# Kernel optimization log

Measured on AMD Instinct MI355X. Metric: run time of the kernel, lower is better.

The kernel has to match this reference:

```python
import jax, jax.numpy as jnp
import numpy as np

N, E = 50000, 800000
IN_F, OUT_F, HID, MSG = 64, 64, 128, 64
TAU = 0.1
EPS = 1e-10


def setup_inputs() -> dict:
    key = jax.random.key(0)
    ks = jax.random.split(key, 16)
    s = 0.05
    return {
        "x": jax.random.normal(ks[0], (N, IN_F), jnp.float32),
        "z": jax.random.normal(ks[1], (N, OUT_F), jnp.float32),
        "src": jax.random.randint(ks[2], (E,), 0, N, jnp.int32),
        "dst": jax.random.randint(ks[3], (E,), 0, N, jnp.int32),
        "u": jax.random.uniform(ks[4], (E, MSG), jnp.float32),
        # f_enc: Linear(in,hid) -> ReLU -> Linear(hid,msg)
        "W_enc1": jax.random.normal(ks[5], (IN_F, HID), jnp.float32) * s,
        "b_enc1": jnp.zeros((HID,), jnp.float32),
        "W_enc2": jax.random.normal(ks[6], (HID, MSG), jnp.float32) * s,
        "b_enc2": jnp.zeros((MSG,), jnp.float32),
        # f_dec: Linear(msg,hid) -> ReLU
        "W_dec": jax.random.normal(ks[7], (MSG, HID), jnp.float32) * s,
        "b_dec": jnp.zeros((HID,), jnp.float32),
        # GRUCell(in+hid -> out): torch layout [3*out, in_dim], gate order r,z,n
        "W_ih": jax.random.normal(ks[8], (3 * OUT_F, IN_F + HID), jnp.float32) * s,
        "b_ih": jnp.zeros((3 * OUT_F,), jnp.float32),
        "W_hh": jax.random.normal(ks[9], (3 * OUT_F, OUT_F), jnp.float32) * s,
        "b_hh": jnp.zeros((3 * OUT_F,), jnp.float32),
    }


def gru_cell(inp, h, W_ih, b_ih, W_hh, b_hh):
    gi = inp @ W_ih.T + b_ih  # [N, 3*out]
    gh = h @ W_hh.T + b_hh
    i_r, i_z, i_n = jnp.split(gi, 3, axis=-1)
    h_r, h_z, h_n = jnp.split(gh, 3, axis=-1)
    r = jax.nn.sigmoid(i_r + h_r)
    zg = jax.nn.sigmoid(i_z + h_z)
    n = jnp.tanh(i_n + r * h_n)
    return (1.0 - zg) * n + zg * h


def reference(x, z, src, dst, u, W_enc1, b_enc1, W_enc2, b_enc2,
              W_dec, b_dec, W_ih, b_ih, W_hh, b_hh):
    # --- message: gather src features, encode, gumbel-softmax (soft) ---
    src_x = x[src]                                    # [E, in]
    logits = jax.nn.relu(src_x @ W_enc1 + b_enc1) @ W_enc2 + b_enc2  # [E, msg]
    g = -jnp.log(-jnp.log(u + EPS) + EPS)             # gumbel noise
    m = jax.nn.softmax((logits + g) / TAU, axis=-1)   # [E, msg]
    # --- aggregate: per-destination max over mailbox ---
    y = jax.ops.segment_max(m, dst, num_segments=N)   # [N, msg]
    y = jnp.where(jnp.isfinite(y), y, 0.0)            # zero-in-degree -> 0 (DGL default)
    # --- decode + GRU update ---
    dec = jax.nn.relu(y @ W_dec + b_dec)              # [N, hid]
    h_out = gru_cell(jnp.concatenate((x, dec), axis=1), z, W_ih, b_ih, W_hh, b_hh)
    return (h_out, h_out)
```

## Files before the change

### kernel.cpp

```cpp
#include <hip/hip_runtime.h>
#include <stdint.h>

#define N_NODES 50000
#define E_EDGES 800000

typedef float f32x4 __attribute__((ext_vector_type(4)));
typedef short s16x8 __attribute__((ext_vector_type(8)));
typedef unsigned short u16x8 __attribute__((ext_vector_type(8)));

__device__ inline unsigned short f2bf(float f) {
    unsigned int u = __float_as_uint(f);
    return (unsigned short)((u + 0x7FFFu + ((u >> 16) & 1u)) >> 16);
}

__device__ inline f32x4 mfma16(s16x8 a, s16x8 b, f32x4 c) {
    return __builtin_amdgcn_mfma_f32_16x16x32_bf16(a, b, c, 0, 0, 0);
}

__global__ void convert_weights(const float* __restrict__ W_enc1, const float* __restrict__ W_enc2,
                                const float* __restrict__ W_dec, const float* __restrict__ W_ih,
                                const float* __restrict__ W_hh, short* __restrict__ wf) {
    int i = blockIdx.x * 256 + threadIdx.x;
    if (i >= 73728) return;
    int j = i & 7, lane = (i >> 3) & 63, g = i >> 9;
    int l15 = lane & 15, q = lane >> 4;
    float v;
    if (g < 16) {
        int gg = g, kk = gg & 1, t = gg >> 1;
        int n = t * 16 + l15, k = kk * 32 + q * 8 + j;
        v = W_enc1[k * 128 + n];
    } else if (g < 32) {
        int gg = g - 16, kk = gg & 3, t = gg >> 2;
        int n = t * 16 + l15, k = kk * 32 + q * 8 + j;
        v = W_enc2[k * 64 + n];
    } else if (g < 48) {
        int gg = g - 32, kk = gg & 1, t = gg >> 1;
        int n = t * 16 + l15, k = kk * 32 + q * 8 + j;
        v = W_dec[k * 128 + n];
    } else if (g < 120) {
        int gg = g - 48, kk = gg % 6, t = gg / 6;
        int n = t * 16 + l15, k = kk * 32 + q * 8 + j;
        v = W_ih[n * 192 + k];
    } else {
        int gg = g - 120, kk = gg & 1, t = gg >> 1;
        int n = t * 16 + l15, k = kk * 32 + q * 8 + j;
        v = W_hh[n * 64 + k];
    }
    wf[i] = f2bf(v);
}

__global__ __launch_bounds__(256) void encoder_kernel(
    const float* __restrict__ x, const float* __restrict__ bs1, const float* __restrict__ bs2,
    const short* __restrict__ W1f, const short* __restrict__ W2f,
    unsigned short* __restrict__ lgb, float* __restrict__ y) {
    __shared__ short sA[64 * 66];
    __shared__ short sH[64 * 130];
    const int tid = threadIdx.x;
    const int nbase = blockIdx.x * 64;

    {
        int nl = tid >> 2, ch = tid & 3;
        int node = nbase + nl;
        short* dp = sA + nl * 66 + ch * 16;
        if (node < N_NODES) {
            const float4* xr = (const float4*)(x + (size_t)node * 64 + ch * 16);
#pragma unroll
            for (int i = 0; i < 4; ++i) {
                float4 v = xr[i];
                dp[i * 4 + 0] = f2bf(v.x); dp[i * 4 + 1] = f2bf(v.y);
                dp[i * 4 + 2] = f2bf(v.z); dp[i * 4 + 3] = f2bf(v.w);
            }
        } else {
#pragma unroll
            for (int i = 0; i < 16; ++i) dp[i] = 0;
        }
    }
    __syncthreads();

    const int lane = tid & 63, wid = tid >> 6;
    const int quad = lane >> 4, l15 = lane & 15;

    f32x4 acc1[4][2];
#pragma unroll
    for (int m = 0; m < 4; ++m)
#pragma unroll
        for (int tt = 0; tt < 2; ++tt) acc1[m][tt] = (f32x4){0.f, 0.f, 0.f, 0.f};
#pragma unroll
    for (int kk = 0; kk < 2; ++kk) {
        s16x8 b0 = *(const s16x8*)(W1f + (((2 * wid + 0) * 2 + kk) * 64 + lane) * 8);
        s16x8 b1 = *(const s16x8*)(W1f + (((2 * wid + 1) * 2 + kk) * 64 + lane) * 8);
#pragma unroll
        for (int m = 0; m < 4; ++m) {
            s16x8 a = *(const s16x8*)(sA + (m * 16 + l15) * 66 + kk * 32 + quad * 8);
            acc1[m][0] = mfma16(a, b0, acc1[m][0]);
            acc1[m][1] = mfma16(a, b1, acc1[m][1]);
        }
    }
#pragma unroll
    for (int tt = 0; tt < 2; ++tt) {
        int col = (2 * wid + tt) * 16 + l15;
        float bias = bs1[col];
#pragma unroll
        for (int m = 0; m < 4; ++m)
#pragma unroll
            for (int r = 0; r < 4; ++r) {
                float h = fmaxf(acc1[m][tt][r] + bias, 0.f);
                sH[(m * 16 + quad * 4 + r) * 130 + col] = f2bf(h);
            }
    }
    __syncthreads();

    f32x4 acc2[4];
#pragma unroll
    for (int m = 0; m < 4; ++m) acc2[m] = (f32x4){0.f, 0.f, 0.f, 0.f};
#pragma unroll
    for (int kk = 0; kk < 4; ++kk) {
        s16x8 b = *(const s16x8*)(W2f + ((wid * 4 + kk) * 64 + lane) * 8);
#pragma unroll
        for (int m = 0; m < 4; ++m) {
            s16x8 a = *(const s16x8*)(sH + (m * 16 + l15) * 130 + kk * 32 + quad * 8);
            acc2[m] = mfma16(a, b, acc2[m]);
        }
    }
    {
        int col = wid * 16 + l15;
        float bias = bs2[col];
#pragma unroll
        for (int m = 0; m < 4; ++m)
#pragma unroll
            for (int r = 0; r < 4; ++r) {
                int node = nbase + m * 16 + quad * 4 + r;
                if (node < N_NODES) {
                    lgb[(size_t)node * 64 + col] = f2bf(acc2[m][r] + bias);
                    y[(size_t)node * 64 + col] = 0.f;
                }
            }
    }
}

__global__ __launch_bounds__(256) void gumbel_kernel(
    const unsigned short* __restrict__ lgb, const int* __restrict__ src,
    const int* __restrict__ dst, const float* __restrict__ u, float* __restrict__ y) {
    const int tid = threadIdx.x;
    const int l7 = tid & 7;
    const int group = tid >> 3;

    for (int it = blockIdx.x; it < E_EDGES / 32; it += gridDim.x) {
        int e = it * 32 + group;
        int s = src[e];
        int d = dst[e];
        u16x8 lgv = ((const u16x8*)lgb)[(size_t)s * 8 + l7];
        float4 u0 = ((const float4*)u)[(size_t)e * 16 + l7 * 2 + 0];
        float4 u1 = ((const float4*)u)[(size_t)e * 16 + l7 * 2 + 1];
        float uv[8] = {u0.x, u0.y, u0.z, u0.w, u1.x, u1.y, u1.z, u1.w};
        float sc[8];
#pragma unroll
        for (int j = 0; j < 8; ++j) {
            float lg = __uint_as_float((unsigned)lgv[j] << 16);
            float t = -0.69314718f * __builtin_amdgcn_logf(uv[j] + 1e-10f);
            sc[j] = fmaf(14.4269504f, lg, -10.0f * __builtin_amdgcn_logf(t + 1e-10f));
        }
        float mx = sc[0];
#pragma unroll
        for (int j = 1; j < 8; ++j) mx = fmaxf(mx, sc[j]);
#pragma unroll
        for (int m = 1; m < 8; m <<= 1) mx = fmaxf(mx, __shfl_xor(mx, m));
        float sum = 0.f;
#pragma unroll
        for (int j = 0; j < 8; ++j) {
            sc[j] = __builtin_amdgcn_exp2f(sc[j] - mx);
            sum += sc[j];
        }
#pragma unroll
        for (int m = 1; m < 8; m <<= 1) sum += __shfl_xor(sum, m);
        float inv = 1.0f / sum;
        float* yrow = y + (size_t)d * 64 + l7 * 8;
#pragma unroll
        for (int j = 0; j < 8; ++j) {
            float mv = sc[j] * inv;
            if (mv > 1e-3f) {
                atomicMax((int*)(yrow + j), __float_as_int(mv));
            }
        }
    }
}

__global__ __launch_bounds__(256) void node_kernel(
    const float* __restrict__ x, const float* __restrict__ z, const float* __restrict__ y,
    const float* __restrict__ b_dec, const float* __restrict__ b_ih, const float* __restrict__ b_hh,
    const short* __restrict__ Wdf, const short* __restrict__ Wihf, const short* __restrict__ Whhf,
    float* __restrict__ out) {
    __shared__ short sInp[64 * 194];
    __shared__ short sY[64 * 66];
    __shared__ short sZ[64 * 66];

    const int tid = threadIdx.x;
    const int nbase = blockIdx.x * 64;

    {
        int nl = tid >> 2, ch = tid & 3;
        int node = nbase + nl;
        short* dx = sInp + nl * 194 + ch * 16;
        short* dy = sY + nl * 66 + ch * 16;
        short* dz = sZ + nl * 66 + ch * 16;
        if (node < N_NODES) {
            const float4* xr = (const float4*)(x + (size_t)node * 64 + ch * 16);
            const float4* yr = (const float4*)(y + (size_t)node * 64 + ch * 16);
            const float4* zr = (const float4*)(z + (size_t)node * 64 + ch * 16);
#pragma unroll
            for (int i = 0; i < 4; ++i) {
                float4 v = xr[i];
                dx[i * 4 + 0] = f2bf(v.x); dx[i * 4 + 1] = f2bf(v.y);
                dx[i * 4 + 2] = f2bf(v.z); dx[i * 4 + 3] = f2bf(v.w);
                float4 w = yr[i];
                dy[i * 4 + 0] = f2bf(w.x); dy[i * 4 + 1] = f2bf(w.y);
                dy[i * 4 + 2] = f2bf(w.z); dy[i * 4 + 3] = f2bf(w.w);
                float4 q = zr[i];
                dz[i * 4 + 0] = f2bf(q.x); dz[i * 4 + 1] = f2bf(q.y);
                dz[i * 4 + 2] = f2bf(q.z); dz[i * 4 + 3] = f2bf(q.w);
            }
        } else {
#pragma unroll
            for (int i = 0; i < 16; ++i) { dx[i] = 0; dy[i] = 0; dz[i] = 0; }
        }
    }
    __syncthreads();

    const int lane = tid & 63, wid = tid >> 6;
    const int quad = lane >> 4, l15 = lane & 15;

    f32x4 accD[4][2];
#pragma unroll
    for (int m = 0; m < 4; ++m)
#pragma unroll
        for (int tt = 0; tt < 2; ++tt) accD[m][tt] = (f32x4){0.f, 0.f, 0.f, 0.f};
#pragma unroll
    for (int kk = 0; kk < 2; ++kk) {
        s16x8 b0 = *(const s16x8*)(Wdf + (((2 * wid + 0) * 2 + kk) * 64 + lane) * 8);
        s16x8 b1 = *(const s16x8*)(Wdf + (((2 * wid + 1) * 2 + kk) * 64 + lane) * 8);
#pragma unroll
        for (int m = 0; m < 4; ++m) {
            s16x8 a = *(const s16x8*)(sY + (m * 16 + l15) * 66 + kk * 32 + quad * 8);
            accD[m][0] = mfma16(a, b0, accD[m][0]);
            accD[m][1] = mfma16(a, b1, accD[m][1]);
        }
    }
#pragma unroll
    for (int tt = 0; tt < 2; ++tt) {
        int col = (2 * wid + tt) * 16 + l15;
        float bias = b_dec[col];
#pragma unroll
        for (int m = 0; m < 4; ++m)
#pragma unroll
            for (int r = 0; r < 4; ++r) {
                float h = fmaxf(accD[m][tt][r] + bias, 0.f);
                sInp[(m * 16 + quad * 4 + r) * 194 + 64 + col] = f2bf(h);
            }
    }
    __syncthreads();

    f32x4 accI[4][3];
#pragma unroll
    for (int m = 0; m < 4; ++m)
#pragma unroll
        for (int g = 0; g < 3; ++g) accI[m][g] = (f32x4){0.f, 0.f, 0.f, 0.f};
#pragma unroll
    for (int kk = 0; kk < 6; ++kk) {
        s16x8 b0 = *(const s16x8*)(Wihf + (((wid + 0) * 6 + kk) * 64 + lane) * 8);
        s16x8 b1 = *(const s16x8*)(Wihf + (((wid + 4) * 6 + kk) * 64 + lane) * 8);
        s16x8 b2 = *(const s16x8*)(Wihf + (((wid + 8) * 6 + kk) * 64 + lane) * 8);
#pragma unroll
        for (int m = 0; m < 4; ++m) {
            s16x8 a = *(const s16x8*)(sInp + (m * 16 + l15) * 194 + kk * 32 + quad * 8);
            accI[m][0] = mfma16(a, b0, accI[m][0]);
            accI[m][1] = mfma16(a, b1, accI[m][1]);
            accI[m][2] = mfma16(a, b2, accI[m][2]);
        }
    }
    f32x4 accH[4][3];
#pragma unroll
    for (int m = 0; m < 4; ++m)
#pragma unroll
        for (int g = 0; g < 3; ++g) accH[m][g] = (f32x4){0.f, 0.f, 0.f, 0.f};
#pragma unroll
    for (int kk = 0; kk < 2; ++kk) {
        s16x8 b0 = *(const s16x8*)(Whhf + (((wid + 0) * 2 + kk) * 64 + lane) * 8);
        s16x8 b1 = *(const s16x8*)(Whhf + (((wid + 4) * 2 + kk) * 64 + lane) * 8);
        s16x8 b2 = *(const s16x8*)(Whhf + (((wid + 8) * 2 + kk) * 64 + lane) * 8);
#pragma unroll
        for (int m = 0; m < 4; ++m) {
            s16x8 a = *(const s16x8*)(sZ + (m * 16 + l15) * 66 + kk * 32 + quad * 8);
            accH[m][0] = mfma16(a, b0, accH[m][0]);
            accH[m][1] = mfma16(a, b1, accH[m][1]);
            accH[m][2] = mfma16(a, b2, accH[m][2]);
        }
    }

    {
        int j0 = wid * 16 + l15;
        float bir = b_ih[j0], biz = b_ih[64 + j0], bin = b_ih[128 + j0];
        float bhr = b_hh[j0], bhz = b_hh[64 + j0], bhn = b_hh[128 + j0];
#pragma unroll
        for (int m = 0; m < 4; ++m)
#pragma unroll
            for (int r = 0; r < 4; ++r) {
                int node = nbase + m * 16 + quad * 4 + r;
                if (node < N_NODES) {
                    float ir = accI[m][0][r] + bir;
                    float iz = accI[m][1][r] + biz;
                    float in_ = accI[m][2][r] + bin;
                    float hr = accH[m][0][r] + bhr;
                    float hz = accH[m][1][r] + bhz;
                    float hn = accH[m][2][r] + bhn;
                    float rr = 1.f / (1.f + __expf(-(ir + hr)));
                    float zg = 1.f / (1.f + __expf(-(iz + hz)));
                    float e2 = __expf(2.f * (in_ + rr * hn));
                    float nn = 1.f - 2.f / (e2 + 1.f);
                    float hp = z[(size_t)node * 64 + j0];
                    float o = (1.f - zg) * nn + zg * hp;
                    out[(size_t)node * 64 + j0] = o;
                    out[(size_t)(N_NODES + node) * 64 + j0] = o;
                }
            }
    }
}

extern "C" void kernel_launch(void* const* d_in, const int* in_sizes, int n_in,
                              void* d_out, int out_size, void* d_ws, size_t ws_size,
                              hipStream_t stream) {
    const float* x      = (const float*)d_in[0];
    const float* z      = (const float*)d_in[1];
    const int*   src    = (const int*)d_in[2];
    const int*   dst    = (const int*)d_in[3];
    const float* u      = (const float*)d_in[4];
    const float* W_enc1 = (const float*)d_in[5];
    const float* b_enc1 = (const float*)d_in[6];
    const float* W_enc2 = (const float*)d_in[7];
    const float* b_enc2 = (const float*)d_in[8];
    const float* W_dec  = (const float*)d_in[9];
    const float* b_dec  = (const float*)d_in[10];
    const float* W_ih   = (const float*)d_in[11];
    const float* b_ih   = (const float*)d_in[12];
    const float* W_hh   = (const float*)d_in[13];
    const float* b_hh   = (const float*)d_in[14];

    float* out = (float*)d_out;
    float* y = out + (size_t)N_NODES * 64;

    short* wf   = (short*)d_ws;
    short* W1f  = wf;
    short* W2f  = W1f + 8192;
    short* Wdf  = W2f + 8192;
    short* Wihf = Wdf + 8192;
    short* Whhf = Wihf + 36864;
    unsigned short* lgb = (unsigned short*)(Whhf + 12288);

    convert_weights<<<288, 256, 0, stream>>>(W_enc1, W_enc2, W_dec, W_ih, W_hh, wf);
    encoder_kernel<<<(N_NODES + 63) / 64, 256, 0, stream>>>(x, b_enc1, b_enc2, W1f, W2f, lgb, y);
    gumbel_kernel<<<3125, 256, 0, stream>>>(lgb, src, dst, u, y);
    node_kernel<<<(N_NODES + 63) / 64, 256, 0, stream>>>(x, z, y, b_dec, b_ih, b_hh,
                                                         Wdf, Wihf, Whhf, out);
}
```

Before: 123.0 us.

## Restructure gumbel kernel: stage edge indices in LDS, prefetch gathers and nontemporal u loads

The gumbel kernel is reworked so each block handles a fixed 256-edge tile. It stages src/dst indices in shared memory, issues all eight logit gathers up front and software-pipelines the nontemporal loads of u. This adds memory-level parallelism and keeps the streaming u tensor from polluting cache. The encoder now zeroes y with vectorized float4 stores while loading x rather than with scalar stores in the epilogue. The GRU epilogue reads the previous hidden state from the bf16 copy in shared memory instead of global fp32, which lowers precision of the z term. The gumbel launch grid must now match E/256 blocks, and that launch code is not shown.

```diff
diff --git a/kernel.cpp b/kernel.cpp
--- a/kernel.cpp
+++ b/kernel.cpp
@@ -11,6 +11,10 @@
 __device__ inline unsigned short f2bf(float f) {
     unsigned int u = __float_as_uint(f);
     return (unsigned short)((u + 0x7FFFu + ((u >> 16) & 1u)) >> 16);
+}
+
+__device__ inline float bf2f(unsigned short s) {
+    return __uint_as_float((unsigned)s << 16);
 }
 
 __device__ inline f32x4 mfma16(s16x8 a, s16x8 b, f32x4 c) {
@@ -64,11 +68,14 @@
         short* dp = sA + nl * 66 + ch * 16;
         if (node < N_NODES) {
             const float4* xr = (const float4*)(x + (size_t)node * 64 + ch * 16);
+            float4* yw = (float4*)(y + (size_t)node * 64 + ch * 16);
+            const float4 z4 = {0.f, 0.f, 0.f, 0.f};
 #pragma unroll
             for (int i = 0; i < 4; ++i) {
                 float4 v = xr[i];
                 dp[i * 4 + 0] = f2bf(v.x); dp[i * 4 + 1] = f2bf(v.y);
                 dp[i * 4 + 2] = f2bf(v.z); dp[i * 4 + 3] = f2bf(v.w);
+                yw[i] = z4;
             }
         } else {
 #pragma unroll
@@ -130,10 +137,7 @@
 #pragma unroll
             for (int r = 0; r < 4; ++r) {
                 int node = nbase + m * 16 + quad * 4 + r;
-                if (node < N_NODES) {
-                    lgb[(size_t)node * 64 + col] = f2bf(acc2[m][r] + bias);
-                    y[(size_t)node * 64 + col] = 0.f;
-                }
+                if (node < N_NODES) lgb[(size_t)node * 64 + col] = f2bf(acc2[m][r] + bias);
             }
     }
 }
@@ -141,22 +145,41 @@
 __global__ __launch_bounds__(256) void gumbel_kernel(
     const unsigned short* __restrict__ lgb, const int* __restrict__ src,
     const int* __restrict__ dst, const float* __restrict__ u, float* __restrict__ y) {
+    __shared__ int sSrc[256];
+    __shared__ int sDst[256];
     const int tid = threadIdx.x;
     const int l7 = tid & 7;
     const int group = tid >> 3;
-
-    for (int it = blockIdx.x; it < E_EDGES / 32; it += gridDim.x) {
-        int e = it * 32 + group;
-        int s = src[e];
-        int d = dst[e];
-        u16x8 lgv = ((const u16x8*)lgb)[(size_t)s * 8 + l7];
-        float4 u0 = ((const float4*)u)[(size_t)e * 16 + l7 * 2 + 0];
-        float4 u1 = ((const float4*)u)[(size_t)e * 16 + l7 * 2 + 1];
-        float uv[8] = {u0.x, u0.y, u0.z, u0.w, u1.x, u1.y, u1.z, u1.w};
+    const int ebase = blockIdx.x * 256;
+
+    sSrc[tid] = src[ebase + tid];
+    sDst[tid] = dst[ebase + tid];
+    __syncthreads();
+
+    u16x8 lgv[8];
+#pragma unroll
+    for (int i = 0; i < 8; ++i) {
+        int s = sSrc[i * 32 + group];
+        lgv[i] = ((const u16x8*)lgb)[(size_t)s * 8 + l7];
+    }
+    f32x4 ua, ub, ua1, ub1;
+    {
+        const f32x4* up = (const f32x4*)(u + (size_t)(ebase + group) * 64) + l7 * 2;
+        ua = __builtin_nontemporal_load(up);
+        ub = __builtin_nontemporal_load(up + 1);
+    }
+#pragma unroll
+    for (int i = 0; i < 8; ++i) {
+        if (i < 7) {
+            const f32x4* up = (const f32x4*)(u + (size_t)(ebase + (i + 1) * 32 + group) * 64) + l7 * 2;
+            ua1 = __builtin_nontemporal_load(up);
+            ub1 = __builtin_nontemporal_load(up + 1);
+        }
+        float uv[8] = {ua.x, ua.y, ua.z, ua.w, ub.x, ub.y, ub.z, ub.w};
         float sc[8];
 #pragma unroll
         for (int j = 0; j < 8; ++j) {
-            float lg = __uint_as_float((unsigned)lgv[j] << 16);
+            float lg = bf2f((unsigned short)lgv[i][j]);
             float t = -0.69314718f * __builtin_amdgcn_logf(uv[j] + 1e-10f);
             sc[j] = fmaf(14.4269504f, lg, -10.0f * __builtin_amdgcn_logf(t + 1e-10f));
         }
@@ -174,6 +197,7 @@
 #pragma unroll
         for (int m = 1; m < 8; m <<= 1) sum += __shfl_xor(sum, m);
         float inv = 1.0f / sum;
+        int d = sDst[i * 32 + group];
         float* yrow = y + (size_t)d * 64 + l7 * 8;
 #pragma unroll
         for (int j = 0; j < 8; ++j) {
@@ -182,6 +206,7 @@
                 atomicMax((int*)(yrow + j), __float_as_int(mv));
             }
         }
+        ua = ua1; ub = ub1;
     }
 }
 
@@ -316,7 +341,7 @@
                     float zg = 1.f / (1.f + __expf(-(iz + hz)));
                     float e2 = __expf(2.f * (in_ + rr * hn));
                     float nn = 1.f - 2.f / (e2 + 1.f);
-                    float hp = z[(size_t)node * 64 + j0];
+                    float hp = bf2f((unsigned short)sZ[(m * 16 + quad * 4 + r) * 66 + j0]);
                     float o = (1.f - zg) * nn + zg * hp;
                     out[(size_t)node * 64 + j0] = o;
                     out[(size_t)(N_NODES + node) * 64 + j0] = o;
```

Measured after the change: 125.6 us. 1.02x slower.

## Load y and z fragments directly from global in node kernel, swizzle LDS

Applied to the files above, without the earlier changes.

The node kernel no longer stages y and z in shared memory. MFMA A-fragments are now loaded straight from global fp32 and converted with packed bf16 conversion instructions. The x/dec staging buffer uses an XOR swizzle to avoid LDS bank conflicts, and the r/z accumulators for the input and hidden GEMMs are merged to save registers, with launch bounds set for occupancy 4. Zeroing of y moves to vectorized float4 stores in the encoder prologue. The trade-off is redundant global reads of y and z across waves in place of one staged load.

```diff
diff --git a/kernel.cpp b/kernel.cpp
--- a/kernel.cpp
+++ b/kernel.cpp
@@ -11,6 +11,32 @@
 __device__ inline unsigned short f2bf(float f) {
     unsigned int u = __float_as_uint(f);
     return (unsigned short)((u + 0x7FFFu + ((u >> 16) & 1u)) >> 16);
+}
+
+__device__ inline float bf2f(unsigned short s) {
+    return __uint_as_float((unsigned)s << 16);
+}
+
+__device__ inline unsigned cvt_pk(float lo, float hi) {
+    unsigned r;
+    asm("v_cvt_pk_bf16_f32 %0, %1, %2" : "=v"(r) : "v"(lo), "v"(hi));
+    return r;
+}
+
+union U8 {
+    unsigned w[4];
+    s16x8 v;
+};
+
+__device__ inline s16x8 load_frag_f32(const float* base) {
+    float4 a = ((const float4*)base)[0];
+    float4 b = ((const float4*)base)[1];
+    U8 u;
+    u.w[0] = cvt_pk(a.x, a.y);
+    u.w[1] = cvt_pk(a.z, a.w);
+    u.w[2] = cvt_pk(b.x, b.y);
+    u.w[3] = cvt_pk(b.z, b.w);
+    return u.v;
 }
 
 __device__ inline f32x4 mfma16(s16x8 a, s16x8 b, f32x4 c) {
@@ -64,11 +90,14 @@
         short* dp = sA + nl * 66 + ch * 16;
         if (node < N_NODES) {
             const float4* xr = (const float4*)(x + (size_t)node * 64 + ch * 16);
+            float4* yw = (float4*)(y + (size_t)node * 64 + ch * 16);
+            const float4 z4 = {0.f, 0.f, 0.f, 0.f};
 #pragma unroll
             for (int i = 0; i < 4; ++i) {
                 float4 v = xr[i];
                 dp[i * 4 + 0] = f2bf(v.x); dp[i * 4 + 1] = f2bf(v.y);
                 dp[i * 4 + 2] = f2bf(v.z); dp[i * 4 + 3] = f2bf(v.w);
+                yw[i] = z4;
             }
         } else {
 #pragma unroll
@@ -130,10 +159,7 @@
 #pragma unroll
             for (int r = 0; r < 4; ++r) {
                 int node = nbase + m * 16 + quad * 4 + r;
-                if (node < N_NODES) {
-                    lgb[(size_t)node * 64 + col] = f2bf(acc2[m][r] + bias);
-                    y[(size_t)node * 64 + col] = 0.f;
-                }
+                if (node < N_NODES) lgb[(size_t)node * 64 + col] = f2bf(acc2[m][r] + bias);
             }
     }
 }
@@ -156,7 +182,7 @@
         float sc[8];
 #pragma unroll
         for (int j = 0; j < 8; ++j) {
-            float lg = __uint_as_float((unsigned)lgv[j] << 16);
+            float lg = bf2f((unsigned short)lgv[j]);
             float t = -0.69314718f * __builtin_amdgcn_logf(uv[j] + 1e-10f);
             sc[j] = fmaf(14.4269504f, lg, -10.0f * __builtin_amdgcn_logf(t + 1e-10f));
         }
@@ -185,49 +211,40 @@
     }
 }
 
-__global__ __launch_bounds__(256) void node_kernel(
+__global__ __launch_bounds__(256, 4) void node_kernel(
     const float* __restrict__ x, const float* __restrict__ z, const float* __restrict__ y,
     const float* __restrict__ b_dec, const float* __restrict__ b_ih, const float* __restrict__ b_hh,
     const short* __restrict__ Wdf, const short* __restrict__ Wihf, const short* __restrict__ Whhf,
     float* __restrict__ out) {
     __shared__ short sInp[64 * 194];
-    __shared__ short sY[64 * 66];
-    __shared__ short sZ[64 * 66];
 
     const int tid = threadIdx.x;
     const int nbase = blockIdx.x * 64;
+    const int lane = tid & 63, wid = tid >> 6;
+    const int quad = lane >> 4, l15 = lane & 15;
 
     {
         int nl = tid >> 2, ch = tid & 3;
         int node = nbase + nl;
-        short* dx = sInp + nl * 194 + ch * 16;
-        short* dy = sY + nl * 66 + ch * 16;
-        short* dz = sZ + nl * 66 + ch * 16;
+        int h = nl & 7;
+        s16x8* d0 = (s16x8*)(sInp + nl * 194 + (((ch * 2 + 0) ^ h) << 3));
+        s16x8* d1 = (s16x8*)(sInp + nl * 194 + (((ch * 2 + 1) ^ h) << 3));
         if (node < N_NODES) {
             const float4* xr = (const float4*)(x + (size_t)node * 64 + ch * 16);
-            const float4* yr = (const float4*)(y + (size_t)node * 64 + ch * 16);
-            const float4* zr = (const float4*)(z + (size_t)node * 64 + ch * 16);
-#pragma unroll
-            for (int i = 0; i < 4; ++i) {
-                float4 v = xr[i];
-                dx[i * 4 + 0] = f2bf(v.x); dx[i * 4 + 1] = f2bf(v.y);
-                dx[i * 4 + 2] = f2bf(v.z); dx[i * 4 + 3] = f2bf(v.w);
-                float4 w = yr[i];
-                dy[i * 4 + 0] = f2bf(w.x); dy[i * 4 + 1] = f2bf(w.y);
-                dy[i * 4 + 2] = f2bf(w.z); dy[i * 4 + 3] = f2bf(w.w);
-                float4 q = zr[i];
-                dz[i * 4 + 0] = f2bf(q.x); dz[i * 4 + 1] = f2bf(q.y);
-                dz[i * 4 + 2] = f2bf(q.z); dz[i * 4 + 3] = f2bf(q.w);
-            }
+            float4 v0 = xr[0], v1 = xr[1], v2 = xr[2], v3 = xr[3];
+            U8 u0, u1;
+            u0.w[0] = cvt_pk(v0.x, v0.y); u0.w[1] = cvt_pk(v0.z, v0.w);
+            u0.w[2] = cvt_pk(v1.x, v1.y); u0.w[3] = cvt_pk(v1.z, v1.w);
+            u1.w[0] = cvt_pk(v2.x, v2.y); u1.w[1] = cvt_pk(v2.z, v2.w);
+            u1.w[2] = cvt_pk(v3.x, v3.y); u1.w[3] = cvt_pk(v3.z, v3.w);
+            *d0 = u0.v;
+            *d1 = u1.v;
         } else {
-#pragma unroll
-            for (int i = 0; i < 16; ++i) { dx[i] = 0; dy[i] = 0; dz[i] = 0; }
-        }
-    }
-    __syncthreads();
-
-    const int lane = tid & 63, wid = tid >> 6;
-    const int quad = lane >> 4, l15 = lane & 15;
+            s16x8 zz = (s16x8){0, 0, 0, 0, 0, 0, 0, 0};
+            *d0 = zz;
+            *d1 = zz;
+        }
+    }
 
     f32x4 accD[4][2];
 #pragma unroll
@@ -240,30 +257,36 @@
         s16x8 b1 = *(const s16x8*)(Wdf + (((2 * wid + 1) * 2 + kk) * 64 + lane) * 8);
 #pragma unroll
         for (int m = 0; m < 4; ++m) {
-            s16x8 a = *(const s16x8*)(sY + (m * 16 + l15) * 66 + kk * 32 + quad * 8);
+            int row = nbase + m * 16 + l15;
+            if (row > N_NODES - 1) row = N_NODES - 1;
+            s16x8 a = load_frag_f32(y + (size_t)row * 64 + kk * 32 + quad * 8);
             accD[m][0] = mfma16(a, b0, accD[m][0]);
             accD[m][1] = mfma16(a, b1, accD[m][1]);
         }
     }
 #pragma unroll
     for (int tt = 0; tt < 2; ++tt) {
-        int col = (2 * wid + tt) * 16 + l15;
-        float bias = b_dec[col];
+        int col = 64 + (2 * wid + tt) * 16 + l15;
+        float bias = b_dec[col - 64];
 #pragma unroll
         for (int m = 0; m < 4; ++m)
 #pragma unroll
             for (int r = 0; r < 4; ++r) {
-                float h = fmaxf(accD[m][tt][r] + bias, 0.f);
-                sInp[(m * 16 + quad * 4 + r) * 194 + 64 + col] = f2bf(h);
+                float hv = fmaxf(accD[m][tt][r] + bias, 0.f);
+                int row = m * 16 + quad * 4 + r;
+                sInp[row * 194 + (((col >> 3) ^ (row & 7)) << 3) + (col & 7)] = f2bf(hv);
             }
     }
     __syncthreads();
 
-    f32x4 accI[4][3];
-#pragma unroll
-    for (int m = 0; m < 4; ++m)
-#pragma unroll
-        for (int g = 0; g < 3; ++g) accI[m][g] = (f32x4){0.f, 0.f, 0.f, 0.f};
+    f32x4 accRZ[4][2], accIN[4], accHN[4];
+#pragma unroll
+    for (int m = 0; m < 4; ++m) {
+        accRZ[m][0] = (f32x4){0.f, 0.f, 0.f, 0.f};
+        accRZ[m][1] = (f32x4){0.f, 0.f, 0.f, 0.f};
+        accIN[m] = (f32x4){0.f, 0.f, 0.f, 0.f};
+        accHN[m] = (f32x4){0.f, 0.f, 0.f, 0.f};
+    }
 #pragma unroll
     for (int kk = 0; kk < 6; ++kk) {
         s16x8 b0 = *(const s16x8*)(Wihf + (((wid + 0) * 6 + kk) * 64 + lane) * 8);
@@ -271,17 +294,13 @@
         s16x8 b2 = *(const s16x8*)(Wihf + (((wid + 8) * 6 + kk) * 64 + lane) * 8);
 #pragma unroll
         for (int m = 0; m < 4; ++m) {
-            s16x8 a = *(const s16x8*)(sInp + (m * 16 + l15) * 194 + kk * 32 + quad * 8);
-            accI[m][0] = mfma16(a, b0, accI[m][0]);
-            accI[m][1] = mfma16(a, b1, accI[m][1]);
-            accI[m][2] = mfma16(a, b2, accI[m][2]);
-        }
-    }
-    f32x4 accH[4][3];
-#pragma unroll
-    for (int m = 0; m < 4; ++m)
-#pragma unroll
-        for (int g = 0; g < 3; ++g) accH[m][g] = (f32x4){0.f, 0.f, 0.f, 0.f};
+            int row = m * 16 + l15;
+            s16x8 a = *(const s16x8*)(sInp + row * 194 + (((kk * 4 + quad) ^ (row & 7)) << 3));
+            accRZ[m][0] = mfma16(a, b0, accRZ[m][0]);
+            accRZ[m][1] = mfma16(a, b1, accRZ[m][1]);
+            accIN[m] = mfma16(a, b2, accIN[m]);
+        }
+    }
 #pragma unroll
     for (int kk = 0; kk < 2; ++kk) {
         s16x8 b0 = *(const s16x8*)(Whhf + (((wid + 0) * 2 + kk) * 64 + lane) * 8);
@@ -289,31 +308,30 @@
         s16x8 b2 = *(const s16x8*)(Whhf + (((wid + 8) * 2 + kk) * 64 + lane) * 8);
 #pragma unroll
         for (int m = 0; m < 4; ++m) {
-            s16x8 a = *(const s16x8*)(sZ + (m * 16 + l15) * 66 + kk * 32 + quad * 8);
-            accH[m][0] = mfma16(a, b0, accH[m][0]);
-            accH[m][1] = mfma16(a, b1, accH[m][1]);
-            accH[m][2] = mfma16(a, b2, accH[m][2]);
+            int row = nbase + m * 16 + l15;
+            if (row > N_NODES - 1) row = N_NODES - 1;
+            s16x8 a = load_frag_f32(z + (size_t)row * 64 + kk * 32 + quad * 8);
+            accRZ[m][0] = mfma16(a, b0, accRZ[m][0]);
+            accRZ[m][1] = mfma16(a, b1, accRZ[m][1]);
+            accHN[m] = mfma16(a, b2, accHN[m]);
         }
     }
 
     {
         int j0 = wid * 16 + l15;
-        float bir = b_ih[j0], biz = b_ih[64 + j0], bin = b_ih[128 + j0];
-        float bhr = b_hh[j0], bhz = b_hh[64 + j0], bhn = b_hh[128 + j0];
+        float brz0 = b_ih[j0] + b_hh[j0];
+        float brz1 = b_ih[64 + j0] + b_hh[64 + j0];
+        float bin = b_ih[128 + j0], bhn = b_hh[128 + j0];
 #pragma unroll
         for (int m = 0; m < 4; ++m)
 #pragma unroll
             for (int r = 0; r < 4; ++r) {
                 int node = nbase + m * 16 + quad * 4 + r;
                 if (node < N_NODES) {
-                    float ir = accI[m][0][r] + bir;
-                    float iz = accI[m][1][r] + biz;
-                    float in_ = accI[m][2][r] + bin;
-                    float hr = accH[m][0][r] + bhr;
-                    float hz = accH[m][1][r] + bhz;
-                    float hn = accH[m][2][r] + bhn;
-                    float rr = 1.f / (1.f + __expf(-(ir + hr)));
-                    float zg = 1.f / (1.f + __expf(-(iz + hz)));
+                    float rr = 1.f / (1.f + __expf(-(accRZ[m][0][r] + brz0)));
+                    float zg = 1.f / (1.f + __expf(-(accRZ[m][1][r] + brz1)));
+                    float in_ = accIN[m][r] + bin;
+                    float hn = accHN[m][r] + bhn;
                     float e2 = __expf(2.f * (in_ + rr * hn));
                     float nn = 1.f - 2.f / (e2 + 1.f);
                     float hp = z[(size_t)node * 64 + j0];
```

New measurement: 127.8 us. 3.9% more time.
